# Kernel tuning notes

Measured on AMD Instinct MI355X. Metric: run time of the kernel, lower is better.

Reference implementation:

```python
import jax, jax.numpy as jnp
import numpy as np

GAMMA = 0.25      # commitment loss weight (bn.gamma)
STRIDE = 8        # LCCombine upsample stride (embedding rate -> wav rate)
FILTER = 9        # LCCombine local filter size

B, Q, N = 4, 64, 4096
K = 512
C = 256
T = (N - 1) * STRIDE + FILTER - 1  # 32768


def setup_inputs() -> dict:
    key = jax.random.key(0)
    k1, k2, k3, k4, k5 = jax.random.split(key, 5)
    quant_pred = jax.random.normal(k1, (B, C, T), dtype=jnp.float32)
    target_wav = jax.random.randint(k2, (B, T), 0, C, dtype=jnp.int32)
    ze = jax.random.normal(k3, (B, Q, N), dtype=jnp.float32)
    emb = jax.random.normal(k4, (K, Q), dtype=jnp.float32)
    combine_w = jax.random.uniform(k5, (FILTER,), dtype=jnp.float32) / FILTER
    return {"quant_pred": quant_pred, "target_wav": target_wav,
            "ze": ze, "emb": emb, "combine_w": combine_w}


def _lc_combine(x, w):
    # x: (B, 1, N) per-embedding-timestep loss; transposed local conv -> (B, 1, (N-1)*S+F)
    kern = w.reshape(1, 1, FILTER)  # OIH
    return jax.lax.conv_transpose(x, kern, strides=(STRIDE,), padding='VALID',
                                  dimension_numbers=('NCH', 'OIH', 'NCH'))


def reference(quant_pred, target_wav, ze, emb, combine_w):
    sg = jax.lax.stop_gradient
    # pairwise squared L2 distances without the (B,K,Q,N) broadcast:
    # d[b,k,n] = ||ze[b,:,n]||^2 + ||emb[k]||^2 - 2 <ze[b,:,n], emb[k]>
    ze2 = jnp.sum(ze * ze, axis=1)                      # (B, N)
    emb2 = jnp.sum(emb * emb, axis=1)                   # (K,)
    cross = jnp.einsum('bqn,kq->bkn', ze, emb)          # (B, K, N)
    dist = ze2[:, None, :] + emb2[None, :, None] - 2.0 * cross
    ind = jnp.argmin(dist, axis=1)                      # (B, N)
    emb_sel = emb[ind]                                  # (B, N, Q)
    ze_t = jnp.transpose(ze, (0, 2, 1))                 # (B, N, Q)
    # codebook loss: grad to emb only (StopGrad on ze)
    l2_loss_embeds = jnp.sum((sg(ze_t) - emb_sel) ** 2, axis=-1)        # (B, N)
    # commitment loss: grad to ze only (bn.l2norm_min uses sg(emb))
    com_loss_embeds = GAMMA * jnp.sum((ze_t - sg(emb_sel)) ** 2, axis=-1)
    # local-conv combine to wav rate, drop last timestep
    l2_loss_ts = _lc_combine(l2_loss_embeds[:, None, :], combine_w)[..., :-1]   # (B,1,T)
    com_loss_ts = _lc_combine(com_loss_embeds[:, None, :], combine_w)[..., :-1]
    # reconstruction: gathered log-softmax
    log_pred = jax.nn.log_softmax(quant_pred, axis=1)   # (B, C, T)
    log_pred_target = jnp.take_along_axis(log_pred, target_wav[:, None, :], axis=1)  # (B,1,T)
    total_loss_ts = -log_pred_target + l2_loss_ts + com_loss_ts
    return jnp.mean(total_loss_ts)
```

## Files before the change

kernel.cpp:

```cpp
#include <hip/hip_runtime.h>
#include <hip/hip_bf16.h>

static constexpr int Qq = 64, Nn = 4096, Kk = 512, Cc = 256, Tt = 32768;
static constexpr float kLog2e = 1.4426950408889634f;
static constexpr float kLn2 = 0.6931471805599453f;
static constexpr float kInvCount = 1.0f / 131072.0f;

typedef short bf16x8 __attribute__((ext_vector_type(8)));
typedef float f32x4 __attribute__((ext_vector_type(4)));

static __device__ __forceinline__ ushort bf16bits(float f) {
  __hip_bfloat16 h = __float2bfloat16(f);
  return *(ushort*)&h;
}

static __device__ __forceinline__ bf16x8 cvt8(const float* __restrict__ p) {
  float4 a0 = *(const float4*)p;
  float4 a1 = *(const float4*)(p + 4);
  bf16x8 r;
  r[0] = (short)bf16bits(a0.x); r[1] = (short)bf16bits(a0.y);
  r[2] = (short)bf16bits(a0.z); r[3] = (short)bf16bits(a0.w);
  r[4] = (short)bf16bits(a1.x); r[5] = (short)bf16bits(a1.y);
  r[6] = (short)bf16bits(a1.z); r[7] = (short)bf16bits(a1.w);
  return r;
}

__global__ __launch_bounds__(256) void fused_kernel(const float* __restrict__ qp,
                                                    const int* __restrict__ tgt,
                                                    const float* __restrict__ ze,
                                                    const float* __restrict__ emb,
                                                    const float* __restrict__ cw,
                                                    float* __restrict__ part) {
  __shared__ __align__(16) float smem[3456];
  const int tid = threadIdx.x;
  const int bid = blockIdx.x;

  if (bid % 3 == 0) {
    ushort* zs = (ushort*)smem;
    float* e2s = smem + 2304;
    unsigned long long* red = (unsigned long long*)(smem + 2816);

    const int vb = bid / 3;
    const int b = vb >> 6;
    const int n0 = (vb & 63) << 6;
    const float* zebase = ze + (size_t)b * Qq * Nn + n0;

    {
      const int nc = tid & 15;
      const int q0 = tid >> 4;
#pragma unroll
      for (int it = 0; it < 4; ++it) {
        int q = q0 + 16 * it;
        float4 v = *(const float4*)(zebase + (size_t)q * Nn + 4 * nc);
        zs[(4 * nc + 0) * 72 + q] = bf16bits(v.x);
        zs[(4 * nc + 1) * 72 + q] = bf16bits(v.y);
        zs[(4 * nc + 2) * 72 + q] = bf16bits(v.z);
        zs[(4 * nc + 3) * 72 + q] = bf16bits(v.w);
      }
    }
    for (int k = tid; k < Kk; k += 256) {
      const float4* row = (const float4*)(emb + (size_t)k * Qq);
      float a = 0.f;
#pragma unroll
      for (int i = 0; i < 16; ++i) {
        float4 f = row[i];
        a += f.x * f.x + f.y * f.y + f.z * f.z + f.w * f.w;
      }
      e2s[k] = a;
    }
    __syncthreads();

    const int w = tid >> 6, lane = tid & 63;
    const int lc = lane & 15;
    const int lg = lane >> 4;

    bf16x8 bfr[4][2];
#pragma unroll
    for (int ct = 0; ct < 4; ++ct)
#pragma unroll
      for (int ks = 0; ks < 2; ++ks)
        bfr[ct][ks] = *(const bf16x8*)&zs[(ct * 16 + lc) * 72 + ks * 32 + lg * 8];

    unsigned long long pk[4] = {~0ull, ~0ull, ~0ull, ~0ull};
#pragma unroll 2
    for (int mt = 0; mt < 8; ++mt) {
      const int arow = w * 128 + mt * 16 + lc;
      const float* ap = emb + (size_t)arow * Qq;
      f32x4 acc[4] = {{0.f, 0.f, 0.f, 0.f}, {0.f, 0.f, 0.f, 0.f},
                      {0.f, 0.f, 0.f, 0.f}, {0.f, 0.f, 0.f, 0.f}};
#pragma unroll
      for (int ks = 0; ks < 2; ++ks) {
        bf16x8 af = cvt8(ap + ks * 32 + lg * 8);
#pragma unroll
        for (int ct = 0; ct < 4; ++ct)
          acc[ct] = __builtin_amdgcn_mfma_f32_16x16x32_bf16(af, bfr[ct][ks],
                                                            acc[ct], 0, 0, 0);
      }
      const int kbase = w * 128 + mt * 16 + lg * 4;
#pragma unroll
      for (int r = 0; r < 4; ++r) {
        int k = kbase + r;
        float e2v = e2s[k];
#pragma unroll
        for (int ct = 0; ct < 4; ++ct) {
          float sc = e2v - 2.0f * acc[ct][r];
          unsigned u = __float_as_uint(sc);
          u = (u & 0x80000000u) ? ~u : (u | 0x80000000u);
          unsigned long long p = ((unsigned long long)u << 32) | (unsigned)k;
          pk[ct] = (p < pk[ct]) ? p : pk[ct];
        }
      }
    }

#pragma unroll
    for (int ct = 0; ct < 4; ++ct) {
      unsigned long long o = __shfl_xor(pk[ct], 16);
      pk[ct] = (o < pk[ct]) ? o : pk[ct];
      o = __shfl_xor(pk[ct], 32);
      pk[ct] = (o < pk[ct]) ? o : pk[ct];
    }
    if (lane < 16) {
#pragma unroll
      for (int ct = 0; ct < 4; ++ct) red[w * 64 + ct * 16 + lane] = pk[ct];
    }
    __syncthreads();

    if (tid < 64) {
      unsigned long long mn = red[tid];
#pragma unroll
      for (int ww = 1; ww < 4; ++ww) {
        unsigned long long v = red[ww * 64 + tid];
        mn = (v < mn) ? v : mn;
      }
      int kb = (int)(unsigned)(mn & 0xffffffffull);

      const float* zc = zebase + tid;
      const float* er = emb + (size_t)kb * Qq;
      float l2 = 0.f;
#pragma unroll
      for (int q = 0; q < 64; ++q) {
        float d = zc[(size_t)q * Nn] - er[q];
        l2 += d * d;
      }
      float wacc = 0.f;
#pragma unroll
      for (int i = 0; i < 9; ++i) wacc += cw[i];
      if (n0 + tid == Nn - 1) wacc -= cw[0];
      float val = 1.25f * l2 * wacc;
#pragma unroll
      for (int off = 32; off > 0; off >>= 1) val += __shfl_down(val, off);
      if (tid == 0) part[512 + vb] = val;
    }
  } else {
    const int rb = bid - bid / 3 - 1;
    const int col = rb * 256 + tid;
    const int b = col >> 15;
    const int t = col & (Tt - 1);
    const int tg = tgt[col];
    const float* base = qp + (size_t)b * Cc * Tt + t;

    float va[16], vb[16];
    float s0 = 0.f, s1 = 0.f, s2 = 0.f, s3 = 0.f, V = 0.f;

#pragma unroll
    for (int i = 0; i < 16; ++i) va[i] = base[(size_t)i * Tt];

#pragma unroll 1
    for (int c0 = 0; c0 < Cc; c0 += 32) {
#pragma unroll
      for (int i = 0; i < 16; ++i) vb[i] = base[(size_t)(c0 + 16 + i) * Tt];
#pragma unroll
      for (int i = 0; i < 16; ++i) {
        float e = __builtin_amdgcn_exp2f(va[i] * kLog2e);
        if ((i & 3) == 0) s0 += e;
        else if ((i & 3) == 1) s1 += e;
        else if ((i & 3) == 2) s2 += e;
        else s3 += e;
        V = (c0 + i == tg) ? va[i] : V;
      }
      if (c0 + 32 < Cc) {
#pragma unroll
        for (int i = 0; i < 16; ++i) va[i] = base[(size_t)(c0 + 32 + i) * Tt];
      }
#pragma unroll
      for (int i = 0; i < 16; ++i) {
        float e = __builtin_amdgcn_exp2f(vb[i] * kLog2e);
        if ((i & 3) == 0) s0 += e;
        else if ((i & 3) == 1) s1 += e;
        else if ((i & 3) == 2) s2 += e;
        else s3 += e;
        V = (c0 + 16 + i == tg) ? vb[i] : V;
      }
    }
    float S = (s0 + s1) + (s2 + s3);
    float contrib = kLn2 * __builtin_amdgcn_logf(S) - V;

#pragma unroll
    for (int off = 32; off > 0; off >>= 1) contrib += __shfl_down(contrib, off);
    float* wsum = smem + 3328;
    if ((tid & 63) == 0) wsum[tid >> 6] = contrib;
    __syncthreads();
    if (tid == 0) part[rb] = (wsum[0] + wsum[1]) + (wsum[2] + wsum[3]);
  }
}

__global__ __launch_bounds__(256) void final_kernel(const float* __restrict__ part,
                                                    float* __restrict__ out) {
  const int tid = threadIdx.x;
  float s = part[tid] + part[tid + 256] + part[tid + 512];
#pragma unroll
  for (int off = 32; off > 0; off >>= 1) s += __shfl_down(s, off);
  __shared__ float ws[4];
  if ((tid & 63) == 0) ws[tid >> 6] = s;
  __syncthreads();
  if (tid == 0) out[0] = ((ws[0] + ws[1]) + (ws[2] + ws[3])) * kInvCount;
}

extern "C" void kernel_launch(void* const* d_in, const int* in_sizes, int n_in,
                              void* d_out, int out_size, void* d_ws, size_t ws_size,
                              hipStream_t stream) {
  const float* qp  = (const float*)d_in[0];
  const int*   tgt = (const int*)d_in[1];
  const float* ze  = (const float*)d_in[2];
  const float* emb = (const float*)d_in[3];
  const float* cw  = (const float*)d_in[4];
  float* out = (float*)d_out;
  float* part = (float*)d_ws;

  fused_kernel<<<dim3(768), dim3(256), 0, stream>>>(qp, tgt, ze, emb, cw, part);
  final_kernel<<<dim3(1), dim3(256), 0, stream>>>(part, out);
}
```

Measured before the change: 30.92 us.

## Split softmax class dimension across two waves per column to double parallelism

Each log-softmax block now handles 128 columns, with two waves per column group each summing half of the 256 classes. The partial sums and target values are combined through shared memory. The grid grows from 768 to 1280 blocks, interleaving VQ blocks every fifth block, and a min-blocks-per-CU hint is added to launch bounds. The aim is more waves in flight to hide the strided global-load latency, at the cost of an extra sync and shared-memory combine and possible register pressure from the occupancy hint.

```diff
diff --git a/kernel.cpp b/kernel.cpp
--- a/kernel.cpp
+++ b/kernel.cpp
@@ -25,22 +25,20 @@
   return r;
 }
 
-__global__ __launch_bounds__(256) void fused_kernel(const float* __restrict__ qp,
-                                                    const int* __restrict__ tgt,
-                                                    const float* __restrict__ ze,
-                                                    const float* __restrict__ emb,
-                                                    const float* __restrict__ cw,
-                                                    float* __restrict__ part) {
+__global__ __launch_bounds__(256, 5) void fused_kernel(
+    const float* __restrict__ qp, const int* __restrict__ tgt,
+    const float* __restrict__ ze, const float* __restrict__ emb,
+    const float* __restrict__ cw, float* __restrict__ part) {
   __shared__ __align__(16) float smem[3456];
   const int tid = threadIdx.x;
   const int bid = blockIdx.x;
 
-  if (bid % 3 == 0) {
+  if (bid % 5 == 0) {
     ushort* zs = (ushort*)smem;
     float* e2s = smem + 2304;
     unsigned long long* red = (unsigned long long*)(smem + 2816);
 
-    const int vb = bid / 3;
+    const int vb = bid / 5;
     const int b = vb >> 6;
     const int n0 = (vb & 63) << 6;
     const float* zebase = ze + (size_t)b * Qq * Nn + n0;
@@ -149,15 +147,20 @@
       float val = 1.25f * l2 * wacc;
 #pragma unroll
       for (int off = 32; off > 0; off >>= 1) val += __shfl_down(val, off);
-      if (tid == 0) part[512 + vb] = val;
+      if (tid == 0) part[1024 + vb] = val;
     }
   } else {
-    const int rb = bid - bid / 3 - 1;
-    const int col = rb * 256 + tid;
-    const int b = col >> 15;
+    const int rb = bid - bid / 5 - 1;
+    const int col0 = rb * 128;
+    const int b = col0 >> 15;
+    const int l = tid & 63, w = tid >> 6;
+    const int cl = (w >> 1) * 64 + l;
+    const int col = col0 + cl;
     const int t = col & (Tt - 1);
+    const int h = w & 1;
+    const int cb0 = h * 128;
     const int tg = tgt[col];
-    const float* base = qp + (size_t)b * Cc * Tt + t;
+    const float* base = qp + (size_t)b * Cc * Tt + (size_t)cb0 * Tt + t;
 
     float va[16], vb[16];
     float s0 = 0.f, s1 = 0.f, s2 = 0.f, s3 = 0.f, V = 0.f;
@@ -166,7 +169,7 @@
     for (int i = 0; i < 16; ++i) va[i] = base[(size_t)i * Tt];
 
 #pragma unroll 1
-    for (int c0 = 0; c0 < Cc; c0 += 32) {
+    for (int c0 = 0; c0 < 128; c0 += 32) {
 #pragma unroll
       for (int i = 0; i < 16; ++i) vb[i] = base[(size_t)(c0 + 16 + i) * Tt];
 #pragma unroll
@@ -176,9 +179,9 @@
         else if ((i & 3) == 1) s1 += e;
         else if ((i & 3) == 2) s2 += e;
         else s3 += e;
-        V = (c0 + i == tg) ? va[i] : V;
-      }
-      if (c0 + 32 < Cc) {
+        V = (cb0 + c0 + i == tg) ? va[i] : V;
+      }
+      if (c0 + 32 < 128) {
 #pragma unroll
         for (int i = 0; i < 16; ++i) va[i] = base[(size_t)(c0 + 32 + i) * Tt];
       }
@@ -189,25 +192,37 @@
         else if ((i & 3) == 1) s1 += e;
         else if ((i & 3) == 2) s2 += e;
         else s3 += e;
-        V = (c0 + 16 + i == tg) ? vb[i] : V;
+        V = (cb0 + c0 + 16 + i == tg) ? vb[i] : V;
       }
     }
     float S = (s0 + s1) + (s2 + s3);
-    float contrib = kLn2 * __builtin_amdgcn_logf(S) - V;
-
-#pragma unroll
-    for (int off = 32; off > 0; off >>= 1) contrib += __shfl_down(contrib, off);
-    float* wsum = smem + 3328;
-    if ((tid & 63) == 0) wsum[tid >> 6] = contrib;
-    __syncthreads();
-    if (tid == 0) part[rb] = (wsum[0] + wsum[1]) + (wsum[2] + wsum[3]);
+
+    float* ssm = smem;
+    float* vvm = smem + 256;
+    ssm[h * 128 + cl] = S;
+    vvm[h * 128 + cl] = V;
+    __syncthreads();
+
+    float contrib = 0.f;
+    if (tid < 128) {
+      float Sm = ssm[tid] + ssm[128 + tid];
+      float Vm = vvm[tid] + vvm[128 + tid];
+      contrib = kLn2 * __builtin_amdgcn_logf(Sm) - Vm;
+#pragma unroll
+      for (int off = 32; off > 0; off >>= 1) contrib += __shfl_down(contrib, off);
+      if ((tid & 63) == 0) smem[512 + (tid >> 6)] = contrib;
+    }
+    __syncthreads();
+    if (tid == 0) part[rb] = smem[512] + smem[513];
   }
 }
 
 __global__ __launch_bounds__(256) void final_kernel(const float* __restrict__ part,
                                                     float* __restrict__ out) {
   const int tid = threadIdx.x;
-  float s = part[tid] + part[tid + 256] + part[tid + 512];
+  float s = 0.f;
+#pragma unroll
+  for (int i = 0; i < 5; ++i) s += part[tid + 256 * i];
 #pragma unroll
   for (int off = 32; off > 0; off >>= 1) s += __shfl_down(s, off);
   __shared__ float ws[4];
@@ -227,6 +242,6 @@
   float* out = (float*)d_out;
   float* part = (float*)d_ws;
 
-  fused_kernel<<<dim3(768), dim3(256), 0, stream>>>(qp, tgt, ze, emb, cw, part);
+  fused_kernel<<<dim3(1280), dim3(256), 0, stream>>>(qp, tgt, ze, emb, cw, part);
   final_kernel<<<dim3(1), dim3(256), 0, stream>>>(part, out);
 }
```

Result: slower. 34.88 us (+12.8%).
